# Kernel optimization log

Hardware: AMD Instinct MI355X
Metric: run time of the kernel (lower is better)

The kernel has to match this reference:

```python
import jax, jax.numpy as jnp
import numpy as np

B, L, N, D = 256, 200, 512, 64
H = 128  # ode func hidden


def setup_inputs() -> dict:
    key = jax.random.key(0)
    ks = jax.random.split(key, 32)
    f32 = jnp.float32

    def w(k, shape, fan_in):
        return (jax.random.normal(k, shape, f32) / np.float32(np.sqrt(fan_in)))

    inp = {}
    inp["x_seq"] = jax.random.normal(ks[0], (B, L, N), f32)
    inp["tvec"] = jnp.arange(L, dtype=f32) * f32(0.01)  # strictly increasing, uniform
    inp["eps"] = jax.random.normal(ks[1], (B, D), f32)
    # Encoder: n_in->512->256->128, mu/logvar heads 128->D
    inp["e_w1"] = w(ks[2], (N, 512), N);   inp["e_b1"] = jnp.zeros((512,), f32)
    inp["e_w2"] = w(ks[3], (512, 256), 512); inp["e_b2"] = jnp.zeros((256,), f32)
    inp["e_w3"] = w(ks[4], (256, 128), 256); inp["e_b3"] = jnp.zeros((128,), f32)
    inp["mu_w"] = w(ks[5], (128, D), 128); inp["mu_b"] = jnp.zeros((D,), f32)
    inp["lv_w"] = w(ks[6], (128, D), 128); inp["lv_b"] = jnp.zeros((D,), f32)
    # LatentODEFunc: D->128 SiLU ->128 SiLU ->D, LayerNorm(D)
    inp["f1_w1"] = w(ks[7], (D, H), D);   inp["f1_b1"] = jnp.zeros((H,), f32)
    inp["f1_w2"] = w(ks[8], (H, H), H);   inp["f1_b2"] = jnp.zeros((H,), f32)
    inp["f2_w"] = w(ks[9], (H, D), H);    inp["f2_b"] = jnp.zeros((D,), f32)
    inp["ln_g"] = jnp.ones((D,), f32);    inp["ln_b"] = jnp.zeros((D,), f32)
    # Decoder: D->512->512->N
    inp["d_w1"] = w(ks[10], (D, 512), D);   inp["d_b1"] = jnp.zeros((512,), f32)
    inp["d_w2"] = w(ks[11], (512, 512), 512); inp["d_b2"] = jnp.zeros((512,), f32)
    inp["d_w3"] = w(ks[12], (512, N), 512); inp["d_b3"] = jnp.zeros((N,), f32)
    return inp


def reference(x_seq, tvec, eps,
              e_w1, e_b1, e_w2, e_b2, e_w3, e_b3, mu_w, mu_b, lv_w, lv_b,
              f1_w1, f1_b1, f1_w2, f1_b2, f2_w, f2_b, ln_g, ln_b,
              d_w1, d_b1, d_w2, d_b2, d_w3, d_b3):
    # ----- Encoder on x0 -----
    x0 = x_seq[:, 0, :]                                   # [B, N]
    h = jax.nn.relu(x0 @ e_w1 + e_b1)
    h = jax.nn.relu(h @ e_w2 + e_b2)
    h = jax.nn.relu(h @ e_w3 + e_b3)
    mu = h @ mu_w + mu_b                                  # [B, D]
    logvar = h @ lv_w + lv_b                              # [B, D]
    z0 = mu + jnp.exp(0.5 * logvar) * eps                 # reparam

    # ----- LatentODEFunc (t is unused by the module) -----
    def odefunc(z):
        hh = jax.nn.silu(z @ f1_w1 + f1_b1)
        hh = jax.nn.silu(hh @ f1_w2 + f1_b2)
        dz = hh @ f2_w + f2_b
        m = jnp.mean(dz, axis=-1, keepdims=True)
        v = jnp.mean((dz - m) ** 2, axis=-1, keepdims=True)
        return (dz - m) / jnp.sqrt(v + 1e-5) * ln_g + ln_b

    # ----- Fixed-step RK4: step_size = t[1]-t[0]; uniform grid => one step per interval -----
    dt = tvec[1:] - tvec[:-1]                             # [L-1]

    def step(z, h_i):
        k1 = odefunc(z)
        k2 = odefunc(z + 0.5 * h_i * k1)
        k3 = odefunc(z + 0.5 * h_i * k2)
        k4 = odefunc(z + h_i * k3)
        z_next = z + (h_i / 6.0) * (k1 + 2.0 * k2 + 2.0 * k3 + k4)
        return z_next, z_next

    _, zs = jax.lax.scan(step, z0, dt)                    # [L-1, B, D]
    z_traj = jnp.concatenate([z0[None], zs], axis=0)      # [L, B, D]
    z_traj = jnp.transpose(z_traj, (1, 0, 2))             # [B, L, D]

    zdiff = (z_traj[:, 1:, :] - z_traj[:, :-1, :]) / dt.reshape(1, -1, 1)

    # ----- Decoder on full trajectory -----
    g = jax.nn.relu(z_traj @ d_w1 + d_b1)
    g = jax.nn.relu(g @ d_w2 + d_b2)
    xhat = g @ d_w3 + d_b3                                # [B, L, N]
    return xhat, mu, logvar, z_traj, zdiff
```

## Files before the change

kernel.cpp:

```cpp
#include <hip/hip_runtime.h>

typedef unsigned short u16;

#define BB 256
#define LL 200
#define NN 512
#define DD 64
#define HH 128

#define MU_OFF   26214400
#define LV_OFF   26230784
#define ZT_OFF   26247168
#define ZD_OFF   29523968

typedef __attribute__((ext_vector_type(8))) short bf8v;
typedef __attribute__((ext_vector_type(4))) short bf4v;
typedef __attribute__((ext_vector_type(4))) float f32x4;

__device__ __forceinline__ float bf2f(u16 u) {
    union { unsigned int i; float f; } v; v.i = ((unsigned int)u) << 16; return v.f;
}
__device__ __forceinline__ u16 f2bf(float f) {
    union { float f; unsigned int u; } v; v.f = f;
    unsigned int r = v.u + 0x7FFFu + ((v.u >> 16) & 1u);
    return (u16)(r >> 16);
}
__device__ __forceinline__ bool detect_f32(const void* tvec) {
    float v = bf2f(((const u16*)tvec)[199]);
    return !(v > 1.5f && v < 2.5f);
}
__device__ __forceinline__ float loadf(const void* p, long idx, bool f32m) {
    return f32m ? ((const float*)p)[idx] : bf2f(((const u16*)p)[idx]);
}

__global__ __launch_bounds__(512) void enc_kernel(
    const void* __restrict__ x_seq, const void* __restrict__ tvec,
    const void* __restrict__ epsp,
    const void* __restrict__ ew1, const void* __restrict__ eb1,
    const void* __restrict__ ew2, const void* __restrict__ eb2,
    const void* __restrict__ ew3, const void* __restrict__ eb3,
    const void* __restrict__ muw, const void* __restrict__ mub,
    const void* __restrict__ lvw, const void* __restrict__ lvb,
    float* __restrict__ out, float* __restrict__ z0f)
{
    __shared__ __align__(16) float xs[2][512];
    __shared__ __align__(16) float h1[2][512];
    __shared__ __align__(16) float h2[2][256];
    __shared__ __align__(16) float h3[2][128];
    __shared__ float muv[2][64], lvv[2][64];
    const bool m = detect_f32(tvec);
    const int t = threadIdx.x;
    const int b0 = blockIdx.x * 2;

    xs[0][t] = loadf(x_seq, (long)(b0 + 0) * 102400 + t, m);
    xs[1][t] = loadf(x_seq, (long)(b0 + 1) * 102400 + t, m);
    __syncthreads();

    {
        float a0 = 0.f, a1 = 0.f;
        const float4* x0v = (const float4*)xs[0];
        const float4* x1v = (const float4*)xs[1];
        #pragma unroll 4
        for (int j4 = 0; j4 < 128; ++j4) {
            float4 xa = x0v[j4], xb = x1v[j4];
            float w0 = loadf(ew1, (4 * j4 + 0) * 512 + t, m);
            float w1v = loadf(ew1, (4 * j4 + 1) * 512 + t, m);
            float w2v = loadf(ew1, (4 * j4 + 2) * 512 + t, m);
            float w3v = loadf(ew1, (4 * j4 + 3) * 512 + t, m);
            a0 += xa.x * w0 + xa.y * w1v + xa.z * w2v + xa.w * w3v;
            a1 += xb.x * w0 + xb.y * w1v + xb.z * w2v + xb.w * w3v;
        }
        float bb = loadf(eb1, t, m);
        h1[0][t] = fmaxf(a0 + bb, 0.f);
        h1[1][t] = fmaxf(a1 + bb, 0.f);
    }
    __syncthreads();

    {
        const int i = t >> 1, s = t & 1;
        float a0 = 0.f, a1 = 0.f;
        const float4* p0 = (const float4*)&h1[0][s * 256];
        const float4* p1 = (const float4*)&h1[1][s * 256];
        #pragma unroll 4
        for (int j4 = 0; j4 < 64; ++j4) {
            float4 xa = p0[j4], xb = p1[j4];
            int j = s * 256 + 4 * j4;
            float w0 = loadf(ew2, (j + 0) * 256 + i, m);
            float w1v = loadf(ew2, (j + 1) * 256 + i, m);
            float w2v = loadf(ew2, (j + 2) * 256 + i, m);
            float w3v = loadf(ew2, (j + 3) * 256 + i, m);
            a0 += xa.x * w0 + xa.y * w1v + xa.z * w2v + xa.w * w3v;
            a1 += xb.x * w0 + xb.y * w1v + xb.z * w2v + xb.w * w3v;
        }
        a0 += __shfl_xor(a0, 1);
        a1 += __shfl_xor(a1, 1);
        if (s == 0) {
            float bb = loadf(eb2, i, m);
            h2[0][i] = fmaxf(a0 + bb, 0.f);
            h2[1][i] = fmaxf(a1 + bb, 0.f);
        }
    }
    __syncthreads();

    {
        const int i = t >> 2, s = t & 3;
        float a0 = 0.f, a1 = 0.f;
        const float4* p0 = (const float4*)&h2[0][s * 64];
        const float4* p1 = (const float4*)&h2[1][s * 64];
        #pragma unroll 4
        for (int j4 = 0; j4 < 16; ++j4) {
            float4 xa = p0[j4], xb = p1[j4];
            int j = s * 64 + 4 * j4;
            float w0 = loadf(ew3, (j + 0) * 128 + i, m);
            float w1v = loadf(ew3, (j + 1) * 128 + i, m);
            float w2v = loadf(ew3, (j + 2) * 128 + i, m);
            float w3v = loadf(ew3, (j + 3) * 128 + i, m);
            a0 += xa.x * w0 + xa.y * w1v + xa.z * w2v + xa.w * w3v;
            a1 += xb.x * w0 + xb.y * w1v + xb.z * w2v + xb.w * w3v;
        }
        a0 += __shfl_xor(a0, 1); a0 += __shfl_xor(a0, 2);
        a1 += __shfl_xor(a1, 1); a1 += __shfl_xor(a1, 2);
        if (s == 0) {
            float bb = loadf(eb3, i, m);
            h3[0][i] = fmaxf(a0 + bb, 0.f);
            h3[1][i] = fmaxf(a1 + bb, 0.f);
        }
    }
    __syncthreads();

    {
        const int o = t >> 2, s = t & 3;
        const void* wp; const void* bp; int oc;
        if (o < 64) { wp = muw; bp = mub; oc = o; }
        else        { wp = lvw; bp = lvb; oc = o - 64; }
        float a0 = 0.f, a1 = 0.f;
        const float4* p0 = (const float4*)&h3[0][s * 32];
        const float4* p1 = (const float4*)&h3[1][s * 32];
        #pragma unroll
        for (int j4 = 0; j4 < 8; ++j4) {
            float4 xa = p0[j4], xb = p1[j4];
            int j = s * 32 + 4 * j4;
            float w0 = loadf(wp, (j + 0) * 64 + oc, m);
            float w1v = loadf(wp, (j + 1) * 64 + oc, m);
            float w2v = loadf(wp, (j + 2) * 64 + oc, m);
            float w3v = loadf(wp, (j + 3) * 64 + oc, m);
            a0 += xa.x * w0 + xa.y * w1v + xa.z * w2v + xa.w * w3v;
            a1 += xb.x * w0 + xb.y * w1v + xb.z * w2v + xb.w * w3v;
        }
        a0 += __shfl_xor(a0, 1); a0 += __shfl_xor(a0, 2);
        a1 += __shfl_xor(a1, 1); a1 += __shfl_xor(a1, 2);
        if (s == 0) {
            float bb = loadf(bp, oc, m);
            if (o < 64) { muv[0][oc] = a0 + bb; muv[1][oc] = a1 + bb; }
            else        { lvv[0][oc] = a0 + bb; lvv[1][oc] = a1 + bb; }
        }
    }
    __syncthreads();

    if (t < 128) {
        int r = t >> 6, d = t & 63;
        float mm = muv[r][d], l = lvv[r][d];
        float z = mm + expf(0.5f * l) * loadf(epsp, (b0 + r) * 64 + d, m);
        z0f[(b0 + r) * 64 + d] = z;
        out[MU_OFF + (b0 + r) * 64 + d] = mm;
        out[LV_OFF + (b0 + r) * 64 + d] = l;
    }
}

__global__ __launch_bounds__(512) void ode_kernel(
    const void* __restrict__ tvec,
    const void* __restrict__ w1, const void* __restrict__ b1,
    const void* __restrict__ w2, const void* __restrict__ b2,
    const void* __restrict__ w3, const void* __restrict__ b3,
    const void* __restrict__ lng, const void* __restrict__ lnb,
    const float* __restrict__ z0f,
    float* __restrict__ zt_out, float* __restrict__ zd_out)
{
    __shared__ __align__(16) float zc[64];
    __shared__ __align__(16) float h1f[128];
    __shared__ __align__(16) float h2f[128];
    __shared__ float dzf[64];
    __shared__ float dts[200];

    const bool mdt = detect_f32(tvec);
    const int t = threadIdx.x;
    const int b = blockIdx.x;
    const int i1 = t >> 2, s1 = t & 3;
    const int i3 = t >> 3, s3 = t & 7;

    float w1r[16], w2r[32], w3r[16];
    #pragma unroll
    for (int jj = 0; jj < 16; ++jj)
        w1r[jj] = loadf(w1, (16 * s1 + jj) * 128 + i1, mdt);
    #pragma unroll
    for (int jq = 0; jq < 8; ++jq) {
        int base = 32 * s1 + ((4 * jq + 8 * s1) & 31);
        #pragma unroll
        for (int q = 0; q < 4; ++q)
            w2r[jq * 4 + q] = loadf(w2, (base + q) * 128 + i1, mdt);
    }
    #pragma unroll
    for (int jq = 0; jq < 4; ++jq) {
        int base = 16 * s3 + ((4 * jq + 4 * s3) & 15);
        #pragma unroll
        for (int q = 0; q < 4; ++q)
            w3r[jq * 4 + q] = loadf(w3, (base + q) * 64 + i3, mdt);
    }
    const float bias1 = (s1 == 0) ? loadf(b1, i1, mdt) : 0.f;
    const float bias2 = (s1 == 0) ? loadf(b2, i1, mdt) : 0.f;
    const float bias3 = (s3 == 0) ? loadf(b3, i3, mdt) : 0.f;
    float g_ln = 0.f, b_ln = 0.f, zbr = 0.f, kar = 0.f;
    if (t < 64) {
        g_ln = loadf(lng, t, mdt); b_ln = loadf(lnb, t, mdt);
        zbr = z0f[b * 64 + t];
        zc[t] = zbr;
        zt_out[b * 12800 + t] = zbr;
    }
    if (t < 199) dts[t] = loadf(tvec, t + 1, mdt) - loadf(tvec, t, mdt);
    __syncthreads();

    #pragma unroll 1
    for (int step = 0; step < 199; ++step) {
        const float h = dts[step];
        #pragma unroll
        for (int e = 0; e < 4; ++e) {
            float a = 0.f;
            #pragma unroll
            for (int jq = 0; jq < 4; ++jq) {
                float4 zv = *(const float4*)&zc[16 * s1 + 4 * jq];
                a += zv.x * w1r[4 * jq + 0] + zv.y * w1r[4 * jq + 1]
                   + zv.z * w1r[4 * jq + 2] + zv.w * w1r[4 * jq + 3];
            }
            a += __shfl_xor(a, 1); a += __shfl_xor(a, 2);
            if (s1 == 0) { float v = a + bias1; h1f[i1] = v / (1.f + expf(-v)); }
            __syncthreads();

            a = 0.f;
            #pragma unroll
            for (int jq = 0; jq < 8; ++jq) {
                int idx = 32 * s1 + ((4 * jq + 8 * s1) & 31);
                float4 hv = *(const float4*)&h1f[idx];
                a += hv.x * w2r[4 * jq + 0] + hv.y * w2r[4 * jq + 1]
                   + hv.z * w2r[4 * jq + 2] + hv.w * w2r[4 * jq + 3];
            }
            a += __shfl_xor(a, 1); a += __shfl_xor(a, 2);
            if (s1 == 0) { float v = a + bias2; h2f[i1] = v / (1.f + expf(-v)); }
            __syncthreads();

            a = 0.f;
            #pragma unroll
            for (int jq = 0; jq < 4; ++jq) {
                int idx = 16 * s3 + ((4 * jq + 4 * s3) & 15);
                float4 hv = *(const float4*)&h2f[idx];
                a += hv.x * w3r[4 * jq + 0] + hv.y * w3r[4 * jq + 1]
                   + hv.z * w3r[4 * jq + 2] + hv.w * w3r[4 * jq + 3];
            }
            a += __shfl_xor(a, 1); a += __shfl_xor(a, 2); a += __shfl_xor(a, 4);
            if (s3 == 0) dzf[i3] = a + bias3;
            __syncthreads();

            if (t < 64) {
                float v = dzf[t];
                float sm = v;
                #pragma unroll
                for (int mm = 1; mm < 64; mm <<= 1) sm += __shfl_xor(sm, mm);
                float mean = sm * (1.f / 64.f);
                float d = v - mean;
                float sq = d * d;
                #pragma unroll
                for (int mm = 1; mm < 64; mm <<= 1) sq += __shfl_xor(sq, mm);
                float var = sq * (1.f / 64.f);
                float y = d / sqrtf(var + 1e-5f) * g_ln + b_ln;
                if (e == 0)      { kar = y;          zc[t] = zbr + 0.5f * h * y; }
                else if (e == 1) { kar += 2.f * y;   zc[t] = zbr + 0.5f * h * y; }
                else if (e == 2) { kar += 2.f * y;   zc[t] = zbr + h * y; }
                else {
                    kar += y;
                    float zn = zbr + (h * (1.f / 6.f)) * kar;
                    zt_out[b * 12800 + (step + 1) * 64 + t] = zn;
                    zd_out[b * 12736 + step * 64 + t] = (zn - zbr) / h;
                    zbr = zn; zc[t] = zn;
                }
            }
            __syncthreads();
        }
    }
}

__global__ __launch_bounds__(256) void wt_kernel(
    const void* __restrict__ w1, const void* __restrict__ w2,
    const void* __restrict__ w3, const void* __restrict__ tvec,
    u16* __restrict__ wt1, u16* __restrict__ wt2, u16* __restrict__ wt3)
{
    __shared__ u16 tile[64][65];
    const bool m = detect_f32(tvec);
    const int b = blockIdx.x;
    const void* src; u16* dst; int K, kt, nt0;
    if (b < 8)       { src = w1; dst = wt1; K = 64;  kt = 0;          nt0 = b; }
    else if (b < 72) { src = w2; dst = wt2; K = 512; kt = (b-8) >> 3; nt0 = (b-8) & 7; }
    else             { src = w3; dst = wt3; K = 512; kt = (b-72) >> 3; nt0 = (b-72) & 7; }
    const int k0 = kt * 64, n0 = nt0 * 64;
    const int t = threadIdx.x;
    #pragma unroll
    for (int i = 0; i < 16; ++i) {
        int idx = t + 256 * i;
        int r = idx >> 6, c = idx & 63;
        tile[r][c] = f2bf(loadf(src, (long)(k0 + r) * 512 + n0 + c, m));
    }
    __syncthreads();
    #pragma unroll
    for (int i = 0; i < 16; ++i) {
        int idx = t + 256 * i;
        int c = idx >> 6, r = idx & 63;
        int pk = ((r >> 3) & 3) * 16 + ((r >> 5) & 1) * 8 + (r & 7);
        dst[(long)(n0 + c) * K + k0 + pk] = tile[r][c];
    }
}

template<int K, int INROWB, bool RELU, bool TOLDS>
__device__ __forceinline__ void dec_layer(
    const u16* __restrict__ WT, const float* __restrict__ bl,
    const u16* Xin, u16* Xout, float* __restrict__ gout,
    long r0, int w, int lm, int lh)
{
    f32x4 acc[8][4];
    #pragma unroll
    for (int a = 0; a < 8; ++a)
        #pragma unroll
        for (int b = 0; b < 4; ++b) { f32x4 z4 = {0.f, 0.f, 0.f, 0.f}; acc[a][b] = z4; }

    #pragma unroll 1
    for (int kk2 = 0; kk2 < K / 64; ++kk2) {
        #pragma unroll
        for (int half = 0; half < 2; ++half) {
            const int kb = kk2 * 64 + half * 32 + lh * 8;
            bf8v bfr[4];
            #pragma unroll
            for (int mt = 0; mt < 4; ++mt) {
                int mr = mt * 16 + lm;
                int byte = mr * INROWB + kb * 2;
                bfr[mt] = *(const bf8v*)((const char*)Xin + (byte ^ ((mr & 7) << 4)));
            }
            bf8v afr[8];
            #pragma unroll
            for (int nt = 0; nt < 8; ++nt) {
                int n = w * 128 + nt * 16 + lm;
                afr[nt] = *(const bf8v*)&WT[(long)n * K + kk2 * 64 + lh * 16 + half * 8];
            }
            #pragma unroll
            for (int nt = 0; nt < 8; ++nt)
                #pragma unroll
                for (int mt = 0; mt < 4; ++mt)
                    acc[nt][mt] = __builtin_amdgcn_mfma_f32_16x16x32_bf16(
                        afr[nt], bfr[mt], acc[nt][mt], 0, 0, 0);
        }
    }
    __syncthreads();

    #pragma unroll
    for (int nt = 0; nt < 8; ++nt) {
        const int n0 = w * 128 + nt * 16 + lh * 4;
        f32x4 bv = *(const f32x4*)&bl[n0];
        #pragma unroll
        for (int mt = 0; mt < 4; ++mt) {
            f32x4 v = acc[nt][mt];
            v.x += bv.x; v.y += bv.y; v.z += bv.z; v.w += bv.w;
            if (RELU) {
                v.x = fmaxf(v.x, 0.f); v.y = fmaxf(v.y, 0.f);
                v.z = fmaxf(v.z, 0.f); v.w = fmaxf(v.w, 0.f);
            }
            const int mr = mt * 16 + lm;
            if (TOLDS) {
                bf4v h;
                h.x = (short)f2bf(v.x); h.y = (short)f2bf(v.y);
                h.z = (short)f2bf(v.z); h.w = (short)f2bf(v.w);
                int byte = mr * 1024 + n0 * 2;
                *(bf4v*)((char*)Xout + (byte ^ ((mr & 7) << 4))) = h;
            } else {
                *(f32x4*)&gout[(r0 + mr) * 512 + n0] = v;
            }
        }
    }
    __syncthreads();
}

__global__ __launch_bounds__(256, 2) void dec_kernel(
    const float* __restrict__ zt, const void* __restrict__ tvec,
    const u16* __restrict__ wt1, const u16* __restrict__ wt2,
    const u16* __restrict__ wt3,
    const void* __restrict__ b1, const void* __restrict__ b2,
    const void* __restrict__ b3,
    float* __restrict__ xhat)
{
    __shared__ __align__(16) u16 X0[64 * 64];
    __shared__ __align__(16) u16 X1[64 * 512];
    __shared__ __align__(16) float bl1[512], bl2[512], bl3[512];

    const bool m = detect_f32(tvec);
    const int t = threadIdx.x;
    const int l = t & 63, w = t >> 6;
    const int lm = l & 15, lh = l >> 4;
    const long r0 = (long)blockIdx.x * 64;

    bl1[t] = loadf(b1, t, m); bl1[t + 256] = loadf(b1, t + 256, m);
    bl2[t] = loadf(b2, t, m); bl2[t + 256] = loadf(b2, t + 256, m);
    bl3[t] = loadf(b3, t, m); bl3[t + 256] = loadf(b3, t + 256, m);

    {
        const int mrow = t >> 2;
        const int c0 = (t & 3) * 16;
        const float* zr = zt + (r0 + mrow) * 64 + c0;
        #pragma unroll
        for (int j = 0; j < 4; ++j) {
            float4 v = *(const float4*)(zr + 4 * j);
            bf4v h;
            h.x = (short)f2bf(v.x); h.y = (short)f2bf(v.y);
            h.z = (short)f2bf(v.z); h.w = (short)f2bf(v.w);
            int byte = mrow * 128 + (c0 + 4 * j) * 2;
            *(bf4v*)((char*)X0 + (byte ^ ((mrow & 7) << 4))) = h;
        }
    }
    __syncthreads();

    dec_layer< 64,  128, true,  true >(wt1, bl1, X0, X1, nullptr, r0, w, lm, lh);
    dec_layer<512, 1024, true,  true >(wt2, bl2, X1, X1, nullptr, r0, w, lm, lh);
    dec_layer<512, 1024, false, false>(wt3, bl3, X1, nullptr, xhat, r0, w, lm, lh);
}

extern "C" void kernel_launch(void* const* d_in, const int* in_sizes, int n_in,
                              void* d_out, int out_size, void* d_ws, size_t ws_size,
                              hipStream_t stream)
{
    float* out = (float*)d_out;
    float* z0f = (float*)d_ws;
    u16* wt1 = (u16*)((char*)d_ws + 65536);
    u16* wt2 = (u16*)((char*)d_ws + 65536 + 65536);
    u16* wt3 = (u16*)((char*)d_ws + 65536 + 65536 + 524288);

    wt_kernel<<<136, 256, 0, stream>>>(
        d_in[21], d_in[23], d_in[25], d_in[1], wt1, wt2, wt3);

    enc_kernel<<<128, 512, 0, stream>>>(
        d_in[0], d_in[1], d_in[2], d_in[3], d_in[4], d_in[5], d_in[6],
        d_in[7], d_in[8], d_in[9], d_in[10], d_in[11], d_in[12],
        out, z0f);

    ode_kernel<<<256, 512, 0, stream>>>(
        d_in[1], d_in[13], d_in[14], d_in[15], d_in[16],
        d_in[17], d_in[18], d_in[19], d_in[20], z0f,
        out + ZT_OFF, out + ZD_OFF);

    dec_kernel<<<800, 256, 0, stream>>>(
        out + ZT_OFF, d_in[1], wt1, wt2, wt3,
        d_in[22], d_in[24], d_in[26], out);
}
```

Measured before the change: 1.650 ms.

## Batch 16 ODE rows per block and run RK4 MLP on bf16 MFMA

```diff
diff --git a/kernel.cpp b/kernel.cpp
--- a/kernel.cpp
+++ b/kernel.cpp
@@ -31,6 +31,12 @@
 }
 __device__ __forceinline__ float loadf(const void* p, long idx, bool f32m) {
     return f32m ? ((const float*)p)[idx] : bf2f(((const u16*)p)[idx]);
+}
+__device__ __forceinline__ bf4v pack4bf(float a, float b, float c, float d) {
+    bf4v r;
+    r.x = (short)f2bf(a); r.y = (short)f2bf(b);
+    r.z = (short)f2bf(c); r.w = (short)f2bf(d);
+    return r;
 }
 
 __global__ __launch_bounds__(512) void enc_kernel(
@@ -167,7 +173,7 @@
     }
 }
 
-__global__ __launch_bounds__(512) void ode_kernel(
+__global__ __launch_bounds__(256, 1) void ode_kernel(
     const void* __restrict__ tvec,
     const void* __restrict__ w1, const void* __restrict__ b1,
     const void* __restrict__ w2, const void* __restrict__ b2,
@@ -176,110 +182,199 @@
     const float* __restrict__ z0f,
     float* __restrict__ zt_out, float* __restrict__ zd_out)
 {
-    __shared__ __align__(16) float zc[64];
-    __shared__ __align__(16) float h1f[128];
-    __shared__ __align__(16) float h2f[128];
-    __shared__ float dzf[64];
+    __shared__ __align__(16) char Zh[16 * 128];
+    __shared__ __align__(16) char Zl[16 * 128];
+    __shared__ __align__(16) char Hs1[16 * 256];
+    __shared__ __align__(16) char Hs2[16 * 256];
     __shared__ float dts[200];
 
-    const bool mdt = detect_f32(tvec);
+    const bool m = detect_f32(tvec);
     const int t = threadIdx.x;
-    const int b = blockIdx.x;
-    const int i1 = t >> 2, s1 = t & 3;
-    const int i3 = t >> 3, s3 = t & 7;
-
-    float w1r[16], w2r[32], w3r[16];
-    #pragma unroll
-    for (int jj = 0; jj < 16; ++jj)
-        w1r[jj] = loadf(w1, (16 * s1 + jj) * 128 + i1, mdt);
-    #pragma unroll
-    for (int jq = 0; jq < 8; ++jq) {
-        int base = 32 * s1 + ((4 * jq + 8 * s1) & 31);
-        #pragma unroll
-        for (int q = 0; q < 4; ++q)
-            w2r[jq * 4 + q] = loadf(w2, (base + q) * 128 + i1, mdt);
-    }
-    #pragma unroll
-    for (int jq = 0; jq < 4; ++jq) {
-        int base = 16 * s3 + ((4 * jq + 4 * s3) & 15);
-        #pragma unroll
-        for (int q = 0; q < 4; ++q)
-            w3r[jq * 4 + q] = loadf(w3, (base + q) * 64 + i3, mdt);
-    }
-    const float bias1 = (s1 == 0) ? loadf(b1, i1, mdt) : 0.f;
-    const float bias2 = (s1 == 0) ? loadf(b2, i1, mdt) : 0.f;
-    const float bias3 = (s3 == 0) ? loadf(b3, i3, mdt) : 0.f;
-    float g_ln = 0.f, b_ln = 0.f, zbr = 0.f, kar = 0.f;
-    if (t < 64) {
-        g_ln = loadf(lng, t, mdt); b_ln = loadf(lnb, t, mdt);
-        zbr = z0f[b * 64 + t];
-        zc[t] = zbr;
-        zt_out[b * 12800 + t] = zbr;
-    }
-    if (t < 199) dts[t] = loadf(tvec, t + 1, mdt) - loadf(tvec, t, mdt);
+    const int w = t >> 6;
+    const int l = t & 63;
+    const int lm = l & 15;
+    const int lh = l >> 4;
+    const int swz = (lm & 7) << 4;
+    const int r0 = blockIdx.x * 16;
+
+    bf8v a1[2][2];
+    #pragma unroll
+    for (int t2 = 0; t2 < 2; ++t2)
+        #pragma unroll
+        for (int kt = 0; kt < 2; ++kt) {
+            bf8v f;
+            #pragma unroll
+            for (int j = 0; j < 8; ++j)
+                f[j] = (short)f2bf(loadf(w1, (long)(kt * 32 + lh * 8 + j) * 128 + 32 * w + 16 * t2 + lm, m));
+            a1[t2][kt] = f;
+        }
+    bf8v a2[2][4];
+    #pragma unroll
+    for (int t2 = 0; t2 < 2; ++t2)
+        #pragma unroll
+        for (int kt = 0; kt < 4; ++kt) {
+            bf8v f;
+            #pragma unroll
+            for (int j = 0; j < 8; ++j)
+                f[j] = (short)f2bf(loadf(w2, (long)(kt * 32 + lh * 8 + j) * 128 + 32 * w + 16 * t2 + lm, m));
+            a2[t2][kt] = f;
+        }
+    bf8v a3[4][4];
+    #pragma unroll
+    for (int t3 = 0; t3 < 4; ++t3)
+        #pragma unroll
+        for (int kt = 0; kt < 4; ++kt) {
+            bf8v f;
+            #pragma unroll
+            for (int j = 0; j < 8; ++j)
+                f[j] = (short)f2bf(loadf(w3, (long)(kt * 32 + lh * 8 + j) * 64 + 16 * t3 + lm, m));
+            a3[t3][kt] = f;
+        }
+
+    float b1r[8], b2r[8];
+    #pragma unroll
+    for (int t2 = 0; t2 < 2; ++t2)
+        #pragma unroll
+        for (int r = 0; r < 4; ++r) {
+            b1r[t2 * 4 + r] = loadf(b1, 32 * w + 16 * t2 + 4 * lh + r, m);
+            b2r[t2 * 4 + r] = loadf(b2, 32 * w + 16 * t2 + 4 * lh + r, m);
+        }
+    float b3r[16], gr[16], brn[16];
+    #pragma unroll
+    for (int t3 = 0; t3 < 4; ++t3)
+        #pragma unroll
+        for (int r = 0; r < 4; ++r) {
+            int n = 16 * t3 + 4 * lh + r;
+            b3r[t3 * 4 + r] = loadf(b3, n, m);
+            gr[t3 * 4 + r]  = loadf(lng, n, m);
+            brn[t3 * 4 + r] = loadf(lnb, n, m);
+        }
+
+    float zbr[16], kar[16];
+    #pragma unroll
+    for (int t3 = 0; t3 < 4; ++t3) {
+        float4 zv = *(const float4*)&z0f[(long)(r0 + lm) * 64 + 16 * t3 + 4 * lh];
+        zbr[4 * t3 + 0] = zv.x; zbr[4 * t3 + 1] = zv.y;
+        zbr[4 * t3 + 2] = zv.z; zbr[4 * t3 + 3] = zv.w;
+    }
+    {
+        float c0 = zbr[4 * w + 0], c1 = zbr[4 * w + 1], c2 = zbr[4 * w + 2], c3 = zbr[4 * w + 3];
+        float4 o; o.x = c0; o.y = c1; o.z = c2; o.w = c3;
+        *(float4*)&zt_out[(long)(r0 + lm) * 12800 + 16 * w + 4 * lh] = o;
+        u16 h0 = f2bf(c0), h1b = f2bf(c1), h2b = f2bf(c2), h3b = f2bf(c3);
+        bf4v hv; hv.x = (short)h0; hv.y = (short)h1b; hv.z = (short)h2b; hv.w = (short)h3b;
+        bf4v lv = pack4bf(c0 - bf2f(h0), c1 - bf2f(h1b), c2 - bf2f(h2b), c3 - bf2f(h3b));
+        int off = lm * 128 + 32 * w + 8 * lh;
+        *(bf4v*)(Zh + (off ^ swz)) = hv;
+        *(bf4v*)(Zl + (off ^ swz)) = lv;
+    }
+    if (t < 199) dts[t] = loadf(tvec, t + 1, m) - loadf(tvec, t, m);
     __syncthreads();
 
     #pragma unroll 1
     for (int step = 0; step < 199; ++step) {
-        const float h = dts[step];
+        const float hstep = dts[step];
         #pragma unroll
         for (int e = 0; e < 4; ++e) {
-            float a = 0.f;
-            #pragma unroll
-            for (int jq = 0; jq < 4; ++jq) {
-                float4 zv = *(const float4*)&zc[16 * s1 + 4 * jq];
-                a += zv.x * w1r[4 * jq + 0] + zv.y * w1r[4 * jq + 1]
-                   + zv.z * w1r[4 * jq + 2] + zv.w * w1r[4 * jq + 3];
-            }
-            a += __shfl_xor(a, 1); a += __shfl_xor(a, 2);
-            if (s1 == 0) { float v = a + bias1; h1f[i1] = v / (1.f + expf(-v)); }
+            {
+                bf8v zh0 = *(const bf8v*)(Zh + ((lm * 128 +  0 + lh * 16) ^ swz));
+                bf8v zh1 = *(const bf8v*)(Zh + ((lm * 128 + 64 + lh * 16) ^ swz));
+                bf8v zl0 = *(const bf8v*)(Zl + ((lm * 128 +  0 + lh * 16) ^ swz));
+                bf8v zl1 = *(const bf8v*)(Zl + ((lm * 128 + 64 + lh * 16) ^ swz));
+                #pragma unroll
+                for (int t2 = 0; t2 < 2; ++t2) {
+                    f32x4 acc = {0.f, 0.f, 0.f, 0.f};
+                    acc = __builtin_amdgcn_mfma_f32_16x16x32_bf16(a1[t2][0], zh0, acc, 0, 0, 0);
+                    acc = __builtin_amdgcn_mfma_f32_16x16x32_bf16(a1[t2][1], zh1, acc, 0, 0, 0);
+                    acc = __builtin_amdgcn_mfma_f32_16x16x32_bf16(a1[t2][0], zl0, acc, 0, 0, 0);
+                    acc = __builtin_amdgcn_mfma_f32_16x16x32_bf16(a1[t2][1], zl1, acc, 0, 0, 0);
+                    float s0, s1, s2, s3;
+                    { float v = acc.x + b1r[t2 * 4 + 0]; s0 = v / (1.f + expf(-v)); }
+                    { float v = acc.y + b1r[t2 * 4 + 1]; s1 = v / (1.f + expf(-v)); }
+                    { float v = acc.z + b1r[t2 * 4 + 2]; s2 = v / (1.f + expf(-v)); }
+                    { float v = acc.w + b1r[t2 * 4 + 3]; s3 = v / (1.f + expf(-v)); }
+                    int off = lm * 256 + 64 * w + 32 * t2 + 8 * lh;
+                    *(bf4v*)(Hs1 + (off ^ swz)) = pack4bf(s0, s1, s2, s3);
+                }
+            }
             __syncthreads();
 
-            a = 0.f;
-            #pragma unroll
-            for (int jq = 0; jq < 8; ++jq) {
-                int idx = 32 * s1 + ((4 * jq + 8 * s1) & 31);
-                float4 hv = *(const float4*)&h1f[idx];
-                a += hv.x * w2r[4 * jq + 0] + hv.y * w2r[4 * jq + 1]
-                   + hv.z * w2r[4 * jq + 2] + hv.w * w2r[4 * jq + 3];
-            }
-            a += __shfl_xor(a, 1); a += __shfl_xor(a, 2);
-            if (s1 == 0) { float v = a + bias2; h2f[i1] = v / (1.f + expf(-v)); }
+            {
+                bf8v hb[4];
+                #pragma unroll
+                for (int kt = 0; kt < 4; ++kt)
+                    hb[kt] = *(const bf8v*)(Hs1 + ((lm * 256 + kt * 64 + lh * 16) ^ swz));
+                #pragma unroll
+                for (int t2 = 0; t2 < 2; ++t2) {
+                    f32x4 acc = {0.f, 0.f, 0.f, 0.f};
+                    #pragma unroll
+                    for (int kt = 0; kt < 4; ++kt)
+                        acc = __builtin_amdgcn_mfma_f32_16x16x32_bf16(a2[t2][kt], hb[kt], acc, 0, 0, 0);
+                    float s0, s1, s2, s3;
+                    { float v = acc.x + b2r[t2 * 4 + 0]; s0 = v / (1.f + expf(-v)); }
+                    { float v = acc.y + b2r[t2 * 4 + 1]; s1 = v / (1.f + expf(-v)); }
+                    { float v = acc.z + b2r[t2 * 4 + 2]; s2 = v / (1.f + expf(-v)); }
+                    { float v = acc.w + b2r[t2 * 4 + 3]; s3 = v / (1.f + expf(-v)); }
+                    int off = lm * 256 + 64 * w + 32 * t2 + 8 * lh;
+                    *(bf4v*)(Hs2 + (off ^ swz)) = pack4bf(s0, s1, s2, s3);
+                }
+            }
             __syncthreads();
 
-            a = 0.f;
-            #pragma unroll
-            for (int jq = 0; jq < 4; ++jq) {
-                int idx = 16 * s3 + ((4 * jq + 4 * s3) & 15);
-                float4 hv = *(const float4*)&h2f[idx];
-                a += hv.x * w3r[4 * jq + 0] + hv.y * w3r[4 * jq + 1]
-                   + hv.z * w3r[4 * jq + 2] + hv.w * w3r[4 * jq + 3];
-            }
-            a += __shfl_xor(a, 1); a += __shfl_xor(a, 2); a += __shfl_xor(a, 4);
-            if (s3 == 0) dzf[i3] = a + bias3;
-            __syncthreads();
-
-            if (t < 64) {
-                float v = dzf[t];
-                float sm = v;
-                #pragma unroll
-                for (int mm = 1; mm < 64; mm <<= 1) sm += __shfl_xor(sm, mm);
-                float mean = sm * (1.f / 64.f);
-                float d = v - mean;
-                float sq = d * d;
-                #pragma unroll
-                for (int mm = 1; mm < 64; mm <<= 1) sq += __shfl_xor(sq, mm);
-                float var = sq * (1.f / 64.f);
-                float y = d / sqrtf(var + 1e-5f) * g_ln + b_ln;
-                if (e == 0)      { kar = y;          zc[t] = zbr + 0.5f * h * y; }
-                else if (e == 1) { kar += 2.f * y;   zc[t] = zbr + 0.5f * h * y; }
-                else if (e == 2) { kar += 2.f * y;   zc[t] = zbr + h * y; }
-                else {
-                    kar += y;
-                    float zn = zbr + (h * (1.f / 6.f)) * kar;
-                    zt_out[b * 12800 + (step + 1) * 64 + t] = zn;
-                    zd_out[b * 12736 + step * 64 + t] = (zn - zbr) / h;
-                    zbr = zn; zc[t] = zn;
+            {
+                bf8v hc[4];
+                #pragma unroll
+                for (int kt = 0; kt < 4; ++kt)
+                    hc[kt] = *(const bf8v*)(Hs2 + ((lm * 256 + kt * 64 + lh * 16) ^ swz));
+                float dz[16];
+                #pragma unroll
+                for (int t3 = 0; t3 < 4; ++t3) {
+                    f32x4 acc = {0.f, 0.f, 0.f, 0.f};
+                    #pragma unroll
+                    for (int kt = 0; kt < 4; ++kt)
+                        acc = __builtin_amdgcn_mfma_f32_16x16x32_bf16(a3[t3][kt], hc[kt], acc, 0, 0, 0);
+                    dz[4 * t3 + 0] = acc.x + b3r[4 * t3 + 0];
+                    dz[4 * t3 + 1] = acc.y + b3r[4 * t3 + 1];
+                    dz[4 * t3 + 2] = acc.z + b3r[4 * t3 + 2];
+                    dz[4 * t3 + 3] = acc.w + b3r[4 * t3 + 3];
+                }
+                float S = 0.f, SS = 0.f;
+                #pragma unroll
+                for (int i = 0; i < 16; ++i) { S += dz[i]; SS = fmaf(dz[i], dz[i], SS); }
+                S  += __shfl_xor(S, 16);  S  += __shfl_xor(S, 32);
+                SS += __shfl_xor(SS, 16); SS += __shfl_xor(SS, 32);
+                float mean = S * (1.f / 64.f);
+                float var  = SS * (1.f / 64.f) - mean * mean;
+                float rstd = rsqrtf(var + 1e-5f);
+                float zc[16];
+                #pragma unroll
+                for (int i = 0; i < 16; ++i) {
+                    float y = (dz[i] - mean) * rstd * gr[i] + brn[i];
+                    if (e == 0)      { kar[i] = y;          zc[i] = zbr[i] + 0.5f * hstep * y; }
+                    else if (e == 1) { kar[i] += 2.f * y;   zc[i] = zbr[i] + 0.5f * hstep * y; }
+                    else if (e == 2) { kar[i] += 2.f * y;   zc[i] = zbr[i] + hstep * y; }
+                    else             { kar[i] += y;         zc[i] = zbr[i] + (hstep * (1.f / 6.f)) * kar[i]; }
+                }
+                if (e == 3) {
+                    float4 o1, o2;
+                    o1.x = zc[4 * w + 0]; o1.y = zc[4 * w + 1]; o1.z = zc[4 * w + 2]; o1.w = zc[4 * w + 3];
+                    o2.x = (zc[4 * w + 0] - zbr[4 * w + 0]) / hstep;
+                    o2.y = (zc[4 * w + 1] - zbr[4 * w + 1]) / hstep;
+                    o2.z = (zc[4 * w + 2] - zbr[4 * w + 2]) / hstep;
+                    o2.w = (zc[4 * w + 3] - zbr[4 * w + 3]) / hstep;
+                    *(float4*)&zt_out[(long)(r0 + lm) * 12800 + (step + 1) * 64 + 16 * w + 4 * lh] = o1;
+                    *(float4*)&zd_out[(long)(r0 + lm) * 12736 + step * 64 + 16 * w + 4 * lh] = o2;
+                    #pragma unroll
+                    for (int i = 0; i < 16; ++i) zbr[i] = zc[i];
+                }
+                {
+                    float c0 = zc[4 * w + 0], c1 = zc[4 * w + 1], c2 = zc[4 * w + 2], c3 = zc[4 * w + 3];
+                    u16 h0 = f2bf(c0), h1b = f2bf(c1), h2b = f2bf(c2), h3b = f2bf(c3);
+                    bf4v hv; hv.x = (short)h0; hv.y = (short)h1b; hv.z = (short)h2b; hv.w = (short)h3b;
+                    bf4v lv = pack4bf(c0 - bf2f(h0), c1 - bf2f(h1b), c2 - bf2f(h2b), c3 - bf2f(h3b));
+                    int off = lm * 128 + 32 * w + 8 * lh;
+                    *(bf4v*)(Zh + (off ^ swz)) = hv;
+                    *(bf4v*)(Zl + (off ^ swz)) = lv;
                 }
             }
             __syncthreads();
@@ -445,7 +540,7 @@
         d_in[7], d_in[8], d_in[9], d_in[10], d_in[11], d_in[12],
         out, z0f);
 
-    ode_kernel<<<256, 512, 0, stream>>>(
+    ode_kernel<<<16, 256, 0, stream>>>(
         d_in[1], d_in[13], d_in[14], d_in[15], d_in[16],
         d_in[17], d_in[18], d_in[19], d_in[20], z0f,
         out + ZT_OFF, out + ZD_OFF);
```

New measurement: 2.161 ms. 1.31x slower.

## Shrink ODE blocks to 256 threads and fuse layer-3 into LayerNorm wave

Applied to the files above, without the earlier changes.

```diff
diff --git a/kernel.cpp b/kernel.cpp
--- a/kernel.cpp
+++ b/kernel.cpp
@@ -167,7 +167,7 @@
     }
 }
 
-__global__ __launch_bounds__(512) void ode_kernel(
+__global__ __launch_bounds__(256, 1) void ode_kernel(
     const void* __restrict__ tvec,
     const void* __restrict__ w1, const void* __restrict__ b1,
     const void* __restrict__ w2, const void* __restrict__ b2,
@@ -179,44 +179,40 @@
     __shared__ __align__(16) float zc[64];
     __shared__ __align__(16) float h1f[128];
     __shared__ __align__(16) float h2f[128];
-    __shared__ float dzf[64];
     __shared__ float dts[200];
 
-    const bool mdt = detect_f32(tvec);
+    const bool m = detect_f32(tvec);
     const int t = threadIdx.x;
     const int b = blockIdx.x;
-    const int i1 = t >> 2, s1 = t & 3;
-    const int i3 = t >> 3, s3 = t & 7;
-
-    float w1r[16], w2r[32], w3r[16];
-    #pragma unroll
-    for (int jj = 0; jj < 16; ++jj)
-        w1r[jj] = loadf(w1, (16 * s1 + jj) * 128 + i1, mdt);
-    #pragma unroll
-    for (int jq = 0; jq < 8; ++jq) {
-        int base = 32 * s1 + ((4 * jq + 8 * s1) & 31);
-        #pragma unroll
-        for (int q = 0; q < 4; ++q)
-            w2r[jq * 4 + q] = loadf(w2, (base + q) * 128 + i1, mdt);
-    }
-    #pragma unroll
-    for (int jq = 0; jq < 4; ++jq) {
-        int base = 16 * s3 + ((4 * jq + 4 * s3) & 15);
-        #pragma unroll
-        for (int q = 0; q < 4; ++q)
-            w3r[jq * 4 + q] = loadf(w3, (base + q) * 64 + i3, mdt);
-    }
-    const float bias1 = (s1 == 0) ? loadf(b1, i1, mdt) : 0.f;
-    const float bias2 = (s1 == 0) ? loadf(b2, i1, mdt) : 0.f;
-    const float bias3 = (s3 == 0) ? loadf(b3, i3, mdt) : 0.f;
-    float g_ln = 0.f, b_ln = 0.f, zbr = 0.f, kar = 0.f;
+    const int i1 = t >> 1, s1 = t & 1;
+    const int t6 = t & 63;
+
+    float w1r[32];
+    #pragma unroll
+    for (int j = 0; j < 32; ++j)
+        w1r[j] = loadf(w1, (long)(32 * s1 + j) * 128 + i1, m);
+    float w2r[64];
+    #pragma unroll
+    for (int j = 0; j < 64; ++j)
+        w2r[j] = loadf(w2, (long)(64 * s1 + j) * 128 + i1, m);
+    float w3r[128];
+    #pragma unroll
+    for (int j = 0; j < 128; ++j)
+        w3r[j] = loadf(w3, (long)j * 64 + t6, m);
+
+    const float bias1 = loadf(b1, i1, m);
+    const float bias2 = loadf(b2, i1, m);
+    const float bias3 = loadf(b3, t6, m);
+    const float g_ln  = loadf(lng, t6, m);
+    const float b_ln  = loadf(lnb, t6, m);
+
+    float zbr = 0.f, kar = 0.f;
     if (t < 64) {
-        g_ln = loadf(lng, t, mdt); b_ln = loadf(lnb, t, mdt);
         zbr = z0f[b * 64 + t];
         zc[t] = zbr;
         zt_out[b * 12800 + t] = zbr;
     }
-    if (t < 199) dts[t] = loadf(tvec, t + 1, mdt) - loadf(tvec, t, mdt);
+    if (t < 199) dts[t] = loadf(tvec, t + 1, m) - loadf(tvec, t, m);
     __syncthreads();
 
     #pragma unroll 1
@@ -224,43 +220,67 @@
         const float h = dts[step];
         #pragma unroll
         for (int e = 0; e < 4; ++e) {
-            float a = 0.f;
-            #pragma unroll
-            for (int jq = 0; jq < 4; ++jq) {
-                float4 zv = *(const float4*)&zc[16 * s1 + 4 * jq];
-                a += zv.x * w1r[4 * jq + 0] + zv.y * w1r[4 * jq + 1]
-                   + zv.z * w1r[4 * jq + 2] + zv.w * w1r[4 * jq + 3];
-            }
-            a += __shfl_xor(a, 1); a += __shfl_xor(a, 2);
-            if (s1 == 0) { float v = a + bias1; h1f[i1] = v / (1.f + expf(-v)); }
+            {
+                float a0 = 0.f, a1 = 0.f, a2 = 0.f, a3 = 0.f;
+                const float4* zv4 = (const float4*)&zc[32 * s1];
+                #pragma unroll
+                for (int q = 0; q < 2; ++q) {
+                    float4 v0 = zv4[4 * q + 0], v1 = zv4[4 * q + 1];
+                    float4 v2 = zv4[4 * q + 2], v3 = zv4[4 * q + 3];
+                    a0 += v0.x * w1r[16 * q + 0] + v0.y * w1r[16 * q + 1]
+                        + v0.z * w1r[16 * q + 2] + v0.w * w1r[16 * q + 3];
+                    a1 += v1.x * w1r[16 * q + 4] + v1.y * w1r[16 * q + 5]
+                        + v1.z * w1r[16 * q + 6] + v1.w * w1r[16 * q + 7];
+                    a2 += v2.x * w1r[16 * q + 8] + v2.y * w1r[16 * q + 9]
+                        + v2.z * w1r[16 * q + 10] + v2.w * w1r[16 * q + 11];
+                    a3 += v3.x * w1r[16 * q + 12] + v3.y * w1r[16 * q + 13]
+                        + v3.z * w1r[16 * q + 14] + v3.w * w1r[16 * q + 15];
+                }
+                float a = (a0 + a1) + (a2 + a3);
+                a += __shfl_xor(a, 1);
+                if (s1 == 0) { float v = a + bias1; h1f[i1] = v / (1.f + expf(-v)); }
+            }
             __syncthreads();
 
-            a = 0.f;
-            #pragma unroll
-            for (int jq = 0; jq < 8; ++jq) {
-                int idx = 32 * s1 + ((4 * jq + 8 * s1) & 31);
-                float4 hv = *(const float4*)&h1f[idx];
-                a += hv.x * w2r[4 * jq + 0] + hv.y * w2r[4 * jq + 1]
-                   + hv.z * w2r[4 * jq + 2] + hv.w * w2r[4 * jq + 3];
-            }
-            a += __shfl_xor(a, 1); a += __shfl_xor(a, 2);
-            if (s1 == 0) { float v = a + bias2; h2f[i1] = v / (1.f + expf(-v)); }
+            {
+                float a0 = 0.f, a1 = 0.f, a2 = 0.f, a3 = 0.f;
+                const float4* hv4 = (const float4*)&h1f[64 * s1];
+                #pragma unroll
+                for (int q = 0; q < 4; ++q) {
+                    float4 v0 = hv4[4 * q + 0], v1 = hv4[4 * q + 1];
+                    float4 v2 = hv4[4 * q + 2], v3 = hv4[4 * q + 3];
+                    a0 += v0.x * w2r[16 * q + 0] + v0.y * w2r[16 * q + 1]
+                        + v0.z * w2r[16 * q + 2] + v0.w * w2r[16 * q + 3];
+                    a1 += v1.x * w2r[16 * q + 4] + v1.y * w2r[16 * q + 5]
+                        + v1.z * w2r[16 * q + 6] + v1.w * w2r[16 * q + 7];
+                    a2 += v2.x * w2r[16 * q + 8] + v2.y * w2r[16 * q + 9]
+                        + v2.z * w2r[16 * q + 10] + v2.w * w2r[16 * q + 11];
+                    a3 += v3.x * w2r[16 * q + 12] + v3.y * w2r[16 * q + 13]
+                        + v3.z * w2r[16 * q + 14] + v3.w * w2r[16 * q + 15];
+                }
+                float a = (a0 + a1) + (a2 + a3);
+                a += __shfl_xor(a, 1);
+                if (s1 == 0) { float v = a + bias2; h2f[i1] = v / (1.f + expf(-v)); }
+            }
             __syncthreads();
 
-            a = 0.f;
-            #pragma unroll
-            for (int jq = 0; jq < 4; ++jq) {
-                int idx = 16 * s3 + ((4 * jq + 4 * s3) & 15);
-                float4 hv = *(const float4*)&h2f[idx];
-                a += hv.x * w3r[4 * jq + 0] + hv.y * w3r[4 * jq + 1]
-                   + hv.z * w3r[4 * jq + 2] + hv.w * w3r[4 * jq + 3];
-            }
-            a += __shfl_xor(a, 1); a += __shfl_xor(a, 2); a += __shfl_xor(a, 4);
-            if (s3 == 0) dzf[i3] = a + bias3;
-            __syncthreads();
-
             if (t < 64) {
-                float v = dzf[t];
+                float a0 = 0.f, a1 = 0.f, a2 = 0.f, a3 = 0.f;
+                const float4* hv4 = (const float4*)h2f;
+                #pragma unroll
+                for (int q = 0; q < 8; ++q) {
+                    float4 v0 = hv4[4 * q + 0], v1 = hv4[4 * q + 1];
+                    float4 v2 = hv4[4 * q + 2], v3 = hv4[4 * q + 3];
+                    a0 += v0.x * w3r[16 * q + 0] + v0.y * w3r[16 * q + 1]
+                        + v0.z * w3r[16 * q + 2] + v0.w * w3r[16 * q + 3];
+                    a1 += v1.x * w3r[16 * q + 4] + v1.y * w3r[16 * q + 5]
+                        + v1.z * w3r[16 * q + 6] + v1.w * w3r[16 * q + 7];
+                    a2 += v2.x * w3r[16 * q + 8] + v2.y * w3r[16 * q + 9]
+                        + v2.z * w3r[16 * q + 10] + v2.w * w3r[16 * q + 11];
+                    a3 += v3.x * w3r[16 * q + 12] + v3.y * w3r[16 * q + 13]
+                        + v3.z * w3r[16 * q + 14] + v3.w * w3r[16 * q + 15];
+                }
+                float v = (a0 + a1) + (a2 + a3) + bias3;
                 float sm = v;
                 #pragma unroll
                 for (int mm = 1; mm < 64; mm <<= 1) sm += __shfl_xor(sm, mm);
@@ -445,7 +465,7 @@
         d_in[7], d_in[8], d_in[9], d_in[10], d_in[11], d_in[12],
         out, z0f);
 
-    ode_kernel<<<256, 512, 0, stream>>>(
+    ode_kernel<<<256, 256, 0, stream>>>(
         d_in[1], d_in[13], d_in[14], d_in[15], d_in[16],
         d_in[17], d_in[18], d_in[19], d_in[20], z0f,
         out + ZT_OFF, out + ZD_OFF);
```

Result: slower. 2.017 ms (+22.2%).
